# Kernel optimization log

Measured on AMD Instinct MI355X. Metric: run time of the kernel, lower is better.

Reference implementation:

```python
import jax, jax.numpy as jnp
import numpy as np

SAMPLE_POINTS = 1000
THRESH = 0.1
MAX_RATIO = 0.1
BIG = 1e9


def _sobel_boundary(mask):
    # mask: [B, H, W] -> boundary magnitude [B, H, W]
    kx = jnp.array([[-1, 0, 1], [-2, 0, 2], [-1, 0, 1]], jnp.float32).reshape(1, 1, 3, 3)
    ky = jnp.array([[-1, -2, -1], [0, 0, 0], [1, 2, 1]], jnp.float32).reshape(1, 1, 3, 3)
    x = mask[:, None, :, :]
    dn = ('NCHW', 'OIHW', 'NCHW')
    gx = jax.lax.conv_general_dilated(x, kx, (1, 1), [(1, 1), (1, 1)], dimension_numbers=dn)
    gy = jax.lax.conv_general_dilated(x, ky, (1, 1), [(1, 1), (1, 1)], dimension_numbers=dn)
    return jnp.sqrt(gx * gx + gy * gy + 1e-8)[:, 0]


def _extract_points(bmap, keys, H, W):
    # bmap: [B, H, W]. Returns points [B, P, 2] float and validity mask [B, P].
    # Torch version uses torch.where + randperm subsampling; here we pick a
    # uniformly-random subset of valid boundary pixels via noisy top_k
    # (fixed-shape, jit-compatible stream compaction).
    def one(bm, key):
        flat = bm.reshape(-1)
        valid = flat > THRESH
        noise = jax.random.uniform(key, flat.shape)
        score = valid.astype(jnp.float32) * 2.0 + noise  # valid in (2,3), invalid in (0,1)
        _, idx = jax.lax.top_k(score, SAMPLE_POINTS)
        pts = jnp.stack([(idx // W).astype(jnp.float32), (idx % W).astype(jnp.float32)], axis=-1)
        pvalid = valid[idx]
        has_any = valid.any()
        # empty-boundary fallback: single center point (like torch version)
        center = jnp.array([H // 2, W // 2], jnp.float32)
        pts = jnp.where(has_any, pts, jnp.broadcast_to(center, pts.shape))
        pvalid = jnp.where(has_any, pvalid, jnp.arange(SAMPLE_POINTS) == 0)
        return pts, pvalid

    return jax.vmap(one)(bmap, keys)


def _hausdorff(pp, pv, tp, tv, diag):
    # pp: [B,P,2], tp: [B,T,2]; masked symmetric Hausdorff per batch element.
    pp2 = jnp.sum(pp * pp, -1)  # [B,P]
    tp2 = jnp.sum(tp * tp, -1)  # [B,T]
    d2 = pp2[:, :, None] + tp2[:, None, :] - 2.0 * jnp.einsum('bpc,btc->bpt', pp, tp)
    D = jnp.sqrt(jnp.maximum(d2, 0.0))  # [B,P,T]
    min_p2t = jnp.min(jnp.where(tv[:, None, :], D, BIG), axis=2)  # [B,P]
    a = jnp.max(jnp.where(pv, min_p2t, -BIG), axis=1)  # [B]
    min_t2p = jnp.min(jnp.where(pv[:, :, None], D, BIG), axis=1)  # [B,T]
    b = jnp.max(jnp.where(tv, min_t2p, -BIG), axis=1)  # [B]
    hd = jnp.maximum(a, b) / diag
    return jnp.clip(hd, 0.0, MAX_RATIO)


def setup_inputs() -> dict:
    key = jax.random.key(0)
    k1, k2 = jax.random.split(key)
    B, H, W = 64, 512, 512
    pred_logits = jax.random.normal(k1, (B, H, W), dtype=jnp.float32)
    target = (jax.random.uniform(k2, (B, H, W)) > 0.5).astype(jnp.float32)
    return {"pred_logits": pred_logits, "target": target}


def reference(pred_logits, target):
    B, H, W = pred_logits.shape
    pred_probs = jax.nn.sigmoid(pred_logits)
    bmap_pred = _sobel_boundary(pred_probs)
    bmap_tgt = _sobel_boundary(target)
    keys = jax.random.split(jax.random.key(1), 2 * B)
    pp, pv = _extract_points(bmap_pred, keys[:B], H, W)
    tp, tv = _extract_points(bmap_tgt, keys[B:], H, W)
    diag = jnp.sqrt(jnp.float32(H * H + W * W))
    hd = _hausdorff(pp, pv, tp, tv, diag)  # [B]
    return jnp.mean(hd)
```

## Files before the change

kernel.cpp:

```cpp
#include <hip/hip_runtime.h>
#include <stdint.h>


#define HH 512
#define WW 512
#define NPIX (HH * WW)
#define NSEL 1000
#define SLICE_CAP 320
#define CUTM (253u << 14)
#define BITCUT ((((253u << 15) - 1u)) << 9)
#define ROWS_PER 32

#if __has_builtin(__builtin_amdgcn_alignbit)
__device__ __forceinline__ uint32_t rotl32(uint32_t x, int r) {
  return __builtin_amdgcn_alignbit(x, x, (32 - r) & 31);
}
#else
__device__ __forceinline__ uint32_t rotl32(uint32_t x, int r) {
  return (x << r) | (x >> (32 - r));
}
#endif

template <int R>
__device__ __forceinline__ uint32_t rotlT(uint32_t x) {
  uint32_t d;
  asm("v_alignbit_b32 %0, %1, %1, %2" : "=v"(d) : "v"(x), "n"(32 - R));
  return d;
}

__device__ __forceinline__ void tf2x32(uint32_t k0, uint32_t k1,
                                       uint32_t c0, uint32_t c1,
                                       uint32_t& o0, uint32_t& o1) {
  uint32_t ks2 = k0 ^ k1 ^ 0x1BD11BDAu;
  uint32_t x0 = c0 + k0, x1 = c1 + k1;
#define TF_R(r) { x0 += x1; x1 = rotl32(x1, (r)); x1 ^= x0; }
  TF_R(13) TF_R(15) TF_R(26) TF_R(6)
  x0 += k1;  x1 += ks2 + 1u;
  TF_R(17) TF_R(29) TF_R(16) TF_R(24)
  x0 += ks2; x1 += k0 + 2u;
  TF_R(13) TF_R(15) TF_R(26) TF_R(6)
  x0 += k0;  x1 += k1 + 3u;
  TF_R(17) TF_R(29) TF_R(16) TF_R(24)
  x0 += k1;  x1 += ks2 + 4u;
  TF_R(13) TF_R(15) TF_R(26) TF_R(6)
  x0 += ks2; x1 += k0 + 5u;
#undef TF_R
  o0 = x0; o1 = x1;
}

__device__ __forceinline__ uint32_t m_from_bits(uint32_t bits) {
  float noise = __uint_as_float((bits >> 9) | 0x3F800000u) - 1.0f;
  float score = 2.0f + noise;
  return __float_as_uint(score) - 0x40000000u;
}

__device__ __forceinline__ uint32_t pixel_m(uint32_t k0, uint32_t k1, int p) {
  uint32_t b1, b2;
  tf2x32(k0, k1, 0u, (uint32_t)p, b1, b2);
  return m_from_bits(b1 ^ b2);
}

__device__ __forceinline__ float sigf(float x) { return 1.0f / (1.0f + __expf(-x)); }

__device__ __forceinline__ float ldval(const float* __restrict__ img, int r, int c, bool isPred) {
  if (r < 0 || r > HH - 1 || c < 0 || c > WW - 1) return 0.0f;
  float v = img[(size_t)r * WW + c];
  return isPred ? sigf(v) : v;
}

__device__ __forceinline__ uint32_t pack_pt(uint32_t p) {
  return ((p >> 9) << 16) | (p & 511u);
}

template <bool PRED>
__device__ __forceinline__ void sobel_body(const float* __restrict__ img, int b,
                                           int slice, int t,
                                           unsigned long long* stage, int* s_cn,
                                           int* s_cv) {
  const int lane = t & 63, w = t >> 6;
  const int rbase = slice * ROWS_PER + 8 * w;
  uint32_t k0, k1;
  tf2x32(0u, 1u, 0u, (uint32_t)b, k0, k1);
  k0 = __builtin_amdgcn_readfirstlane(k0);
  k1 = __builtin_amdgcn_readfirstlane(k1);
  const uint32_t ks2 = k0 ^ k1 ^ 0x1BD11BDAu;

  float P[10], Q[10], R[10];
  float4 na, nb;
  int cnt = 0;
  const uint32_t pbase = (uint32_t)((rbase << 9) + (lane << 3));

  auto issue = [&](int rn) {
    if ((unsigned)rn < (unsigned)HH) {
      const float* rp = img + ((size_t)rn << 9) + (lane << 3);
      na = *(const float4*)rp;
      nb = *(const float4*)(rp + 4);
    }
  };
  auto promote = [&](float (&vv)[10], int rn) {
    if ((unsigned)rn < (unsigned)HH) {
      float4 x = na, y = nb;
      if (PRED) {
        x.x = sigf(x.x); x.y = sigf(x.y); x.z = sigf(x.z); x.w = sigf(x.w);
        y.x = sigf(y.x); y.y = sigf(y.y); y.z = sigf(y.z); y.w = sigf(y.w);
      }
      vv[1] = x.x; vv[2] = x.y; vv[3] = x.z; vv[4] = x.w;
      vv[5] = y.x; vv[6] = y.y; vv[7] = y.z; vv[8] = y.w;
      float l = __shfl_up(y.w, 1);
      float r = __shfl_down(x.x, 1);
      vv[0] = (lane == 0) ? 0.0f : l;
      vv[9] = (lane == 63) ? 0.0f : r;
    } else {
#pragma unroll
      for (int i = 0; i < 10; ++i) vv[i] = 0.0f;
    }
  };

  issue(rbase - 1); promote(P, rbase - 1);
  issue(rbase);     promote(Q, rbase);
  issue(rbase + 1);

#pragma unroll 1
  for (int r = 0; r < 8; ++r) {
    promote(R, rbase + r + 1);
    if (r < 7) issue(rbase + r + 2);
    __builtin_amdgcn_sched_barrier(0);

    const uint32_t prow = pbase + ((uint32_t)r << 9);
    uint32_t X0[8], X1[8];
    const uint32_t pk = prow + k1;
#pragma unroll
    for (int j = 0; j < 8; ++j) { X0[j] = k0; X1[j] = pk + (uint32_t)j; }
#define RND(rr)                                                         \
  _Pragma("unroll") for (int j = 0; j < 8; ++j) {                       \
    X0[j] += X1[j];                                                     \
    X1[j] = rotlT<(rr)>(X1[j]) ^ X0[j];                                 \
  }
#define INJ(ka, kb, i)                                                  \
  _Pragma("unroll") for (int j = 0; j < 8; ++j) {                       \
    X0[j] += (ka);                                                      \
    X1[j] += (kb) + (uint32_t)(i);                                      \
  }
    RND(13) RND(15) RND(26) RND(6)  INJ(k1, ks2, 1)
    RND(17) RND(29) RND(16) RND(24) INJ(ks2, k0, 2)
    RND(13) RND(15) RND(26) RND(6)  INJ(k0, k1, 3)
    RND(17) RND(29) RND(16) RND(24) INJ(k1, ks2, 4)
    RND(13) RND(15) RND(26) RND(6)  INJ(ks2, k0, 5)
#undef RND
#undef INJ
    uint32_t bits[8];
#pragma unroll
    for (int j = 0; j < 8; ++j) bits[j] = X0[j] ^ X1[j];

    float da[10], e[10];
#pragma unroll
    for (int k = 0; k < 10; ++k) {
      da[k] = R[k] - P[k];
      e[k] = P[k] + 2.0f * Q[k] + R[k];
    }
    uint32_t candmask = 0;
#pragma unroll
    for (int j = 0; j < 8; ++j) {
      float gx = e[j + 2] - e[j];
      float gy = da[j] + 2.0f * da[j + 1] + da[j + 2];
      bool vld = (gx * gx + gy * gy + 1e-8f) > 0.01f;
      cnt += vld ? 1 : 0;
      candmask |= ((vld && bits[j] >= BITCUT) ? 1u : 0u) << j;
    }
    if (candmask) {
      int base = atomicAdd(s_cn, __popc(candmask));
      do {
        int j = __ffs(candmask) - 1;
        candmask &= candmask - 1;
        if (base < SLICE_CAP) {
          uint32_t m = m_from_bits(bits[j]);
          stage[base] = ((unsigned long long)m << 32) | (prow + (uint32_t)j);
        }
        ++base;
      } while (candmask);
    }
#pragma unroll
    for (int k = 0; k < 10; ++k) { P[k] = Q[k]; Q[k] = R[k]; }
  }
#pragma unroll
  for (int o = 32; o > 0; o >>= 1) cnt += __shfl_down(cnt, o);
  if (lane == 0) atomicAdd(s_cv, cnt);
}

__global__ __launch_bounds__(256, 4) void sobel_cand(
    const float* __restrict__ pred, const float* __restrict__ tgt,
    int2* __restrict__ g_scnt, unsigned long long* __restrict__ g_cand) {
  const int bid = blockIdx.x;
  const int b = bid >> 4, s = bid & 15;
  const int t = threadIdx.x;
  __shared__ unsigned long long stage[SLICE_CAP];
  __shared__ int s_cn, s_cv;
  if (t == 0) { s_cn = 0; s_cv = 0; }
  __syncthreads();
  if (b < 64) sobel_body<true>(pred + (size_t)b * NPIX, b, s, t, stage, &s_cn, &s_cv);
  else        sobel_body<false>(tgt + (size_t)(b - 64) * NPIX, b, s, t, stage, &s_cn, &s_cv);
  __syncthreads();
  const int raw = s_cn;
  const int n = raw < SLICE_CAP ? raw : SLICE_CAP;
  for (int i = t; i < n; i += 256) g_cand[(size_t)bid * SLICE_CAP + i] = stage[i];
  if (t == 0) g_scnt[bid] = make_int2(s_cv, raw);
}

__global__ __launch_bounds__(256) void resolve_kernel(
    const float* __restrict__ pred, const float* __restrict__ tgt,
    const int2* __restrict__ g_scnt, unsigned long long* __restrict__ g_cand,
    uint32_t* __restrict__ g_pts, int* __restrict__ g_counts) {
  const int img = blockIdx.x;
  const int t = threadIdx.x;

  __shared__ unsigned long long cand_s[16 * SLICE_CAP];
  __shared__ int segc[16];
  __shared__ int s_scx[16], s_scy[16];
  __shared__ int s_info[4];
  __shared__ int ch[256];
  __shared__ int fh[1024];
  __shared__ int aux[256];
  __shared__ unsigned long long ties[256];
  __shared__ int s_pos, s_nt, s_T1, s_r1, s_T2, s_r2, s_n;

  if (t < 16) {
    int2 v = g_scnt[img * 16 + t];
    s_scx[t] = v.x; s_scy[t] = v.y;
    segc[t] = v.y < SLICE_CAP ? v.y : SLICE_CAP;
  }
  if (t == 0) { s_pos = 0; s_nt = 0; s_n = 0; }
  __syncthreads();
  if (t == 0) {
    int cv = 0, hi = 0, ovf = 0;
    for (int s = 0; s < 16; ++s) {
      cv += s_scx[s]; hi += s_scy[s];
      if (s_scy[s] > SLICE_CAP) ovf = 1;
    }
    s_info[0] = cv; s_info[1] = hi; s_info[2] = ovf;
  }
  __syncthreads();
  const int cv = s_info[0];
  if (cv == 0) {
    if (t == 0) { g_pts[img * NSEL] = (256u << 16) | 256u; g_counts[img] = 1; }
    return;
  }
  const int need = cv < NSEL ? cv : NSEL;
  bool slow = (s_info[2] != 0) || (s_info[1] < need);

  unsigned long long* C = g_cand + (size_t)img * 16 * SLICE_CAP;
  int ncand = 0;

  if (slow) {
    const bool isPred = img < 64;
    const float* im = isPred ? pred + (size_t)img * NPIX : tgt + (size_t)(img - 64) * NPIX;
    uint32_t k0, k1;
    tf2x32(0u, 1u, 0u, (uint32_t)img, k0, k1);
    ch[t] = 0;
    __syncthreads();
    for (int p = t; p < NPIX; p += 256) {
      int r = p >> 9, c = p & 511;
      float gx = (ldval(im, r - 1, c + 1, isPred) - ldval(im, r - 1, c - 1, isPred)) +
                 2.0f * (ldval(im, r, c + 1, isPred) - ldval(im, r, c - 1, isPred)) +
                 (ldval(im, r + 1, c + 1, isPred) - ldval(im, r + 1, c - 1, isPred));
      float gy = (ldval(im, r + 1, c - 1, isPred) - ldval(im, r - 1, c - 1, isPred)) +
                 2.0f * (ldval(im, r + 1, c, isPred) - ldval(im, r - 1, c, isPred)) +
                 (ldval(im, r + 1, c + 1, isPred) - ldval(im, r - 1, c + 1, isPred));
      if ((gx * gx + gy * gy + 1e-8f) > 0.01f) {
        uint32_t m = pixel_m(k0, k1, p);
        uint32_t cb = m >> 14; if (cb > 255u) cb = 255u;
        atomicAdd(&ch[cb], 1);
      }
    }
    __syncthreads();
    {
      aux[t] = ch[t];
      __syncthreads();
      for (int o = 1; o < 256; o <<= 1) {
        int v = (t + o < 256) ? aux[t + o] : 0;
        __syncthreads();
        aux[t] += v;
        __syncthreads();
      }
      int nx = (t + 1 < 256) ? aux[t + 1] : 0;
      if (aux[t] >= need && nx < need) s_T1 = t;
      __syncthreads();
    }
    const uint32_t Tc = (uint32_t)s_T1;
    if (t == 0) s_info[3] = 0;
    __syncthreads();
    for (int p = t; p < NPIX; p += 256) {
      int r = p >> 9, c = p & 511;
      float gx = (ldval(im, r - 1, c + 1, isPred) - ldval(im, r - 1, c - 1, isPred)) +
                 2.0f * (ldval(im, r, c + 1, isPred) - ldval(im, r, c - 1, isPred)) +
                 (ldval(im, r + 1, c + 1, isPred) - ldval(im, r + 1, c - 1, isPred));
      float gy = (ldval(im, r + 1, c - 1, isPred) - ldval(im, r - 1, c - 1, isPred)) +
                 2.0f * (ldval(im, r + 1, c, isPred) - ldval(im, r - 1, c, isPred)) +
                 (ldval(im, r + 1, c + 1, isPred) - ldval(im, r - 1, c + 1, isPred));
      if ((gx * gx + gy * gy + 1e-8f) > 0.01f) {
        uint32_t m = pixel_m(k0, k1, p);
        uint32_t cb = m >> 14; if (cb > 255u) cb = 255u;
        if (cb >= Tc) {
          int i = atomicAdd(&s_info[3], 1);
          if (i < 16 * SLICE_CAP) C[i] = ((unsigned long long)m << 32) | (uint32_t)p;
        }
      }
    }
    __syncthreads();
    ncand = s_info[3] < 16 * SLICE_CAP ? s_info[3] : 16 * SLICE_CAP;
  }

  if (slow) {
    for (int i = t; i < ncand; i += 256) cand_s[i] = C[i];
    if (t == 0) s_n = ncand;
  } else {
    for (int i = t; i < 16 * SLICE_CAP; i += 256) {
      int s = i / SLICE_CAP;
      int o = i - s * SLICE_CAP;
      if (o < segc[s]) {
        unsigned long long e = C[i];
        cand_s[atomicAdd(&s_n, 1)] = e;
      }
    }
  }
  ch[t] = 0;
  for (int i = t; i < 1024; i += 256) fh[i] = 0;
  __syncthreads();
  const int n = s_n;

  for (int i = t; i < n; i += 256) {
    uint32_t m = (uint32_t)(cand_s[i] >> 32);
    uint32_t cb = m >> 14; if (cb > 255u) cb = 255u;
    atomicAdd(&ch[cb], 1);
  }
  __syncthreads();
  {
    aux[t] = ch[t];
    __syncthreads();
    for (int o = 1; o < 256; o <<= 1) {
      int v = (t + o < 256) ? aux[t + o] : 0;
      __syncthreads();
      aux[t] += v;
      __syncthreads();
    }
    int nx = (t + 1 < 256) ? aux[t + 1] : 0;
    if (aux[t] >= need && nx < need) { s_T1 = t; s_r1 = need - nx; }
    __syncthreads();
  }
  const uint32_t T1 = (uint32_t)s_T1;
  const int r1 = s_r1;
  const uint32_t baseM = T1 << 14;

  for (int i = t; i < n; i += 256) {
    unsigned long long e = cand_s[i];
    uint32_t m = (uint32_t)(e >> 32), p = (uint32_t)e;
    uint32_t cb = m >> 14; if (cb > 255u) cb = 255u;
    if (cb > T1) {
      int pos = atomicAdd(&s_pos, 1);
      g_pts[img * NSEL + pos] = pack_pt(p);
    } else if (cb == T1) {
      uint32_t f = (m - baseM) >> 4; if (f > 1023u) f = 1023u;
      atomicAdd(&fh[f], 1);
    }
  }
  __syncthreads();
  {
    int base = 4 * t, sv = 0;
    for (int j = 3; j >= 0; --j) { sv += fh[base + j]; fh[base + j] = sv; }
    aux[t] = sv;
    __syncthreads();
    for (int o = 1; o < 256; o <<= 1) {
      int v = (t + o < 256) ? aux[t + o] : 0;
      __syncthreads();
      aux[t] += v;
      __syncthreads();
    }
    int add = (t < 255) ? aux[t + 1] : 0;
    for (int j = 0; j < 4; ++j) fh[base + j] += add;
    __syncthreads();
    for (int j = 0; j < 4; ++j) {
      int idx = base + j;
      int sfx = fh[idx];
      int nx = (idx < 1023) ? fh[idx + 1] : 0;
      if (sfx >= r1 && nx < r1) { s_T2 = idx; s_r2 = r1 - nx; }
    }
    __syncthreads();
  }
  const int T2 = s_T2, r2 = s_r2;
  for (int i = t; i < n; i += 256) {
    unsigned long long e = cand_s[i];
    uint32_t m = (uint32_t)(e >> 32), p = (uint32_t)e;
    uint32_t cb = m >> 14; if (cb > 255u) cb = 255u;
    if (cb == T1) {
      uint32_t f = (m - baseM) >> 4; if (f > 1023u) f = 1023u;
      if ((int)f > T2) {
        int pos = atomicAdd(&s_pos, 1);
        g_pts[img * NSEL + pos] = pack_pt(p);
      } else if ((int)f == T2) {
        int j = atomicAdd(&s_nt, 1);
        if (j < 256) ties[j] = e;
      }
    }
  }
  __syncthreads();
  int nt = s_nt < 256 ? s_nt : 256;
  for (int i = t; i < nt; i += 256) {
    unsigned long long e = ties[i];
    uint32_t mi = (uint32_t)(e >> 32), pi = (uint32_t)e;
    int rank = 0;
    for (int j = 0; j < nt; ++j) {
      unsigned long long e2 = ties[j];
      uint32_t mj = (uint32_t)(e2 >> 32), pj = (uint32_t)e2;
      rank += (mj > mi) || (mj == mi && pj < pi);
    }
    if (rank < r2) {
      int pos = atomicAdd(&s_pos, 1);
      g_pts[img * NSEL + pos] = pack_pt(pi);
    }
  }
  __syncthreads();
  if (t == 0) g_counts[img] = s_pos;
}

__global__ __launch_bounds__(256) void haus_kernel(
    const uint32_t* __restrict__ g_pts, const int* __restrict__ g_counts,
    float* __restrict__ g_hpart) {
  const int bid = blockIdx.x;
  const int img = bid >> 3;
  const int dir = (bid >> 2) & 1;
  const int seg = bid & 3;
  const int t = threadIdx.x;
  const int iOwn = dir ? 64 + img : img;
  const int iOth = dir ? img : 64 + img;
  const int nOwn = g_counts[iOwn];
  const int nOth = g_counts[iOth];
  __shared__ float2 o[NSEL];
  __shared__ float red[256];
  for (int i = t; i < nOth; i += 256) {
    uint32_t v = g_pts[iOth * NSEL + i];
    o[i] = make_float2((float)(v >> 16), (float)(v & 0xFFFFu));
  }
  __syncthreads();
  float best = 0.0f;
  const int lo = seg * 250;
  const int hi = min(nOwn, lo + 250);
  for (int i = lo + t; i < hi; i += 256) {
    uint32_t v = g_pts[iOwn * NSEL + i];
    float pr = (float)(v >> 16), pc = (float)(v & 0xFFFFu);
    float mn0 = 3.4e38f, mn1 = 3.4e38f, mn2 = 3.4e38f, mn3 = 3.4e38f;
    int j = 0;
    for (; j + 3 < nOth; j += 4) {
      float dr0 = pr - o[j].x,     dc0 = pc - o[j].y;
      float dr1 = pr - o[j + 1].x, dc1 = pc - o[j + 1].y;
      float dr2 = pr - o[j + 2].x, dc2 = pc - o[j + 2].y;
      float dr3 = pr - o[j + 3].x, dc3 = pc - o[j + 3].y;
      mn0 = fminf(mn0, dr0 * dr0 + dc0 * dc0);
      mn1 = fminf(mn1, dr1 * dr1 + dc1 * dc1);
      mn2 = fminf(mn2, dr2 * dr2 + dc2 * dc2);
      mn3 = fminf(mn3, dr3 * dr3 + dc3 * dc3);
    }
    for (; j < nOth; ++j) {
      float dr = pr - o[j].x, dc = pc - o[j].y;
      mn0 = fminf(mn0, dr * dr + dc * dc);
    }
    float mn = fminf(fminf(mn0, mn1), fminf(mn2, mn3));
    best = fmaxf(best, mn);
  }
  red[t] = best;
  __syncthreads();
  for (int st = 128; st > 0; st >>= 1) {
    if (t < st) red[t] = fmaxf(red[t], red[t + st]);
    __syncthreads();
  }
  if (t == 0) g_hpart[bid] = red[0];
}

__global__ __launch_bounds__(64) void fin_kernel(const float* __restrict__ g_hpart,
                                                 float* __restrict__ out) {
  const int t = threadIdx.x;
  float mx = 0.0f;
  for (int j = 0; j < 8; ++j) mx = fmaxf(mx, g_hpart[t * 8 + j]);
  float diag = sqrtf((float)(HH * HH + WW * WW));
  float hd = sqrtf(fmaxf(mx, 0.0f)) / diag;
  hd = fminf(fmaxf(hd, 0.0f), 0.1f);
  float s = hd;
  for (int o = 32; o > 0; o >>= 1) s += __shfl_down(s, o);
  if (t == 0) out[0] = s * 0.015625f;
}

#define WS_SCNT   0u
#define WS_COUNTS 16384u
#define WS_HPART  (WS_COUNTS + 512u)
#define WS_PTS    (WS_HPART + 2048u)
#define WS_CAND   (WS_PTS + 512000u)

extern "C" void kernel_launch(void* const* d_in, const int* in_sizes, int n_in,
                              void* d_out, int out_size, void* d_ws, size_t ws_size,
                              hipStream_t stream) {
  const float* pred = (const float*)d_in[0];
  const float* tgt = (const float*)d_in[1];
  float* out = (float*)d_out;
  char* ws = (char*)d_ws;
  int2* g_scnt = (int2*)(ws + WS_SCNT);
  int* g_counts = (int*)(ws + WS_COUNTS);
  float* g_hpart = (float*)(ws + WS_HPART);
  uint32_t* g_pts = (uint32_t*)(ws + WS_PTS);
  unsigned long long* g_cand = (unsigned long long*)(ws + WS_CAND);

  sobel_cand<<<2048, 256, 0, stream>>>(pred, tgt, g_scnt, g_cand);
  resolve_kernel<<<128, 256, 0, stream>>>(pred, tgt, g_scnt, g_cand, g_pts, g_counts);
  haus_kernel<<<512, 256, 0, stream>>>(g_pts, g_counts, g_hpart);
  fin_kernel<<<1, 64, 0, stream>>>(g_hpart, out);
}
```

Baseline: 233.3 us.

## Fold final reduction into haus kernel, peel first Threefry round, raise occupancy

Removes the separate final reduction kernel: each Hausdorff block atomically max-reduces its partial into a per-image slot, and the last block, identified by a ticket counter, computes the mean. The slots and counter are zeroed by the first sobel block. The first Threefry round is simplified algebraically because X0 starts as a constant. The sobel kernel's launch bound is raised from 4 to 8 waves per unit, which may force register spills.

```diff
diff --git a/kernel.cpp b/kernel.cpp
--- a/kernel.cpp
+++ b/kernel.cpp
@@ -129,8 +129,13 @@
     const uint32_t prow = pbase + ((uint32_t)r << 9);
     uint32_t X0[8], X1[8];
     const uint32_t pk = prow + k1;
-#pragma unroll
-    for (int j = 0; j < 8; ++j) { X0[j] = k0; X1[j] = pk + (uint32_t)j; }
+    const uint32_t s0 = pk + k0;
+#pragma unroll
+    for (int j = 0; j < 8; ++j) {
+      uint32_t x1i = pk + (uint32_t)j;
+      X0[j] = s0 + (uint32_t)j;
+      X1[j] = rotlT<13>(x1i) ^ X0[j];
+    }
 #define RND(rr)                                                         \
   _Pragma("unroll") for (int j = 0; j < 8; ++j) {                       \
     X0[j] += X1[j];                                                     \
@@ -141,7 +146,7 @@
     X0[j] += (ka);                                                      \
     X1[j] += (kb) + (uint32_t)(i);                                      \
   }
-    RND(13) RND(15) RND(26) RND(6)  INJ(k1, ks2, 1)
+    RND(15) RND(26) RND(6)  INJ(k1, ks2, 1)
     RND(17) RND(29) RND(16) RND(24) INJ(ks2, k0, 2)
     RND(13) RND(15) RND(26) RND(6)  INJ(k0, k1, 3)
     RND(17) RND(29) RND(16) RND(24) INJ(k1, ks2, 4)
@@ -187,15 +192,20 @@
   if (lane == 0) atomicAdd(s_cv, cnt);
 }
 
-__global__ __launch_bounds__(256, 4) void sobel_cand(
+__global__ __launch_bounds__(256, 8) void sobel_cand(
     const float* __restrict__ pred, const float* __restrict__ tgt,
-    int2* __restrict__ g_scnt, unsigned long long* __restrict__ g_cand) {
+    int2* __restrict__ g_scnt, unsigned long long* __restrict__ g_cand,
+    uint32_t* __restrict__ g_hmax, int* __restrict__ g_done) {
   const int bid = blockIdx.x;
   const int b = bid >> 4, s = bid & 15;
   const int t = threadIdx.x;
   __shared__ unsigned long long stage[SLICE_CAP];
   __shared__ int s_cn, s_cv;
   if (t == 0) { s_cn = 0; s_cv = 0; }
+  if (bid == 0) {
+    if (t < 64) g_hmax[t] = 0u;
+    if (t == 64) *g_done = 0;
+  }
   __syncthreads();
   if (b < 64) sobel_body<true>(pred + (size_t)b * NPIX, b, s, t, stage, &s_cn, &s_cv);
   else        sobel_body<false>(tgt + (size_t)(b - 64) * NPIX, b, s, t, stage, &s_cn, &s_cv);
@@ -423,7 +433,8 @@
 
 __global__ __launch_bounds__(256) void haus_kernel(
     const uint32_t* __restrict__ g_pts, const int* __restrict__ g_counts,
-    float* __restrict__ g_hpart) {
+    uint32_t* __restrict__ g_hmax, int* __restrict__ g_done,
+    float* __restrict__ out) {
   const int bid = blockIdx.x;
   const int img = bid >> 3;
   const int dir = (bid >> 2) & 1;
@@ -435,6 +446,7 @@
   const int nOth = g_counts[iOth];
   __shared__ float2 o[NSEL];
   __shared__ float red[256];
+  __shared__ int s_ticket;
   for (int i = t; i < nOth; i += 256) {
     uint32_t v = g_pts[iOth * NSEL + i];
     o[i] = make_float2((float)(v >> 16), (float)(v & 0xFFFFu));
@@ -471,26 +483,31 @@
     if (t < st) red[t] = fmaxf(red[t], red[t + st]);
     __syncthreads();
   }
-  if (t == 0) g_hpart[bid] = red[0];
-}
-
-__global__ __launch_bounds__(64) void fin_kernel(const float* __restrict__ g_hpart,
-                                                 float* __restrict__ out) {
-  const int t = threadIdx.x;
-  float mx = 0.0f;
-  for (int j = 0; j < 8; ++j) mx = fmaxf(mx, g_hpart[t * 8 + j]);
-  float diag = sqrtf((float)(HH * HH + WW * WW));
-  float hd = sqrtf(fmaxf(mx, 0.0f)) / diag;
-  hd = fminf(fmaxf(hd, 0.0f), 0.1f);
-  float s = hd;
-  for (int o = 32; o > 0; o >>= 1) s += __shfl_down(s, o);
-  if (t == 0) out[0] = s * 0.015625f;
+  if (t == 0) {
+    atomicMax(&g_hmax[img], __float_as_uint(red[0]));
+    __threadfence();
+    s_ticket = atomicAdd(g_done, 1);
+  }
+  __syncthreads();
+  if (s_ticket == 511) {
+    __threadfence();
+    if (t < 64) {
+      uint32_t u = atomicMax(&g_hmax[t], 0u);
+      float diag = sqrtf((float)(HH * HH + WW * WW));
+      float hd = sqrtf(fmaxf(__uint_as_float(u), 0.0f)) / diag;
+      hd = fminf(fmaxf(hd, 0.0f), 0.1f);
+      float s = hd;
+      for (int o2 = 32; o2 > 0; o2 >>= 1) s += __shfl_down(s, o2);
+      if (t == 0) out[0] = s * 0.015625f;
+    }
+  }
 }
 
 #define WS_SCNT   0u
 #define WS_COUNTS 16384u
-#define WS_HPART  (WS_COUNTS + 512u)
-#define WS_PTS    (WS_HPART + 2048u)
+#define WS_HMAX   (WS_COUNTS + 512u)
+#define WS_DONE   (WS_HMAX + 256u)
+#define WS_PTS    (WS_HMAX + 2048u)
 #define WS_CAND   (WS_PTS + 512000u)
 
 extern "C" void kernel_launch(void* const* d_in, const int* in_sizes, int n_in,
@@ -502,12 +519,12 @@
   char* ws = (char*)d_ws;
   int2* g_scnt = (int2*)(ws + WS_SCNT);
   int* g_counts = (int*)(ws + WS_COUNTS);
-  float* g_hpart = (float*)(ws + WS_HPART);
+  uint32_t* g_hmax = (uint32_t*)(ws + WS_HMAX);
+  int* g_done = (int*)(ws + WS_DONE);
   uint32_t* g_pts = (uint32_t*)(ws + WS_PTS);
   unsigned long long* g_cand = (unsigned long long*)(ws + WS_CAND);
 
-  sobel_cand<<<2048, 256, 0, stream>>>(pred, tgt, g_scnt, g_cand);
+  sobel_cand<<<2048, 256, 0, stream>>>(pred, tgt, g_scnt, g_cand, g_hmax, g_done);
   resolve_kernel<<<128, 256, 0, stream>>>(pred, tgt, g_scnt, g_cand, g_pts, g_counts);
-  haus_kernel<<<512, 256, 0, stream>>>(g_pts, g_counts, g_hpart);
-  fin_kernel<<<1, 64, 0, stream>>>(g_hpart, out);
-}
+  haus_kernel<<<512, 256, 0, stream>>>(g_pts, g_counts, g_hmax, g_done, out);
+}
```

Result: slower. 245.6 us (+5.3%).
